# Kernel optimization log

Hardware: AMD Instinct MI355X
Metric: run time of the kernel (lower is better)

## Reference

```python
import jax, jax.numpy as jnp
import numpy as np

B, S, DIM = 4, 512, 2048
E, INTER = 32, 1024
G, TOPK_G, TOPK = 8, 4, 6
ROUTE_SCALE = 2.5
SHARED_INTER = 2 * INTER  # n_shared_experts * moe_inter_dim


def setup_inputs() -> dict:
    key = jax.random.key(0)
    ks = jax.random.split(key, 8)
    sd = 0.02
    return {
        "x": jax.random.normal(ks[0], (B, S, DIM), jnp.float32),
        "gate_w": jax.random.normal(ks[1], (E, DIM), jnp.float32) * sd,
        "w11": jax.random.normal(ks[2], (E, INTER, DIM), jnp.float32) * sd,  # gate proj (torch Linear weight [out,in])
        "w33": jax.random.normal(ks[3], (E, INTER, DIM), jnp.float32) * sd,  # up proj
        "w22": jax.random.normal(ks[4], (E, DIM, INTER), jnp.float32) * sd,  # down proj
        "sw1": jax.random.normal(ks[5], (SHARED_INTER, DIM), jnp.float32) * sd,
        "sw2": jax.random.normal(ks[6], (DIM, SHARED_INTER), jnp.float32) * sd,
        "sw3": jax.random.normal(ks[7], (SHARED_INTER, DIM), jnp.float32) * sd,
    }


def _gate(xf, gate_w):
    # sigmoid scores, group-limited greedy top-k (bias=None branch)
    scores = jax.nn.sigmoid(xf @ gate_w.T)                      # [T, E]
    gs = scores.reshape(-1, G, E // G)                          # [T, G, E/G]
    group_scores = gs.max(axis=-1)                              # amax since bias is None
    _, gidx = jax.lax.top_k(group_scores, TOPK_G)               # [T, TOPK_G]
    gmask = jnp.any(jnp.arange(G)[None, None, :] == gidx[:, :, None], axis=1)  # [T, G] keep-mask
    masked = jnp.where(gmask[:, :, None], gs, -jnp.inf).reshape(-1, E)
    _, idx = jax.lax.top_k(masked, TOPK)                        # [T, TOPK]
    w = jnp.take_along_axis(scores, idx, axis=1)                # gather from original (pre-mask) scores
    w = w / jnp.sum(w, axis=-1, keepdims=True) * ROUTE_SCALE    # sigmoid normalization + route_scale
    return w, idx


def reference(x, gate_w, w11, w33, w22, sw1, sw2, sw3):
    xf = x.reshape(-1, DIM)                                     # [T, D]
    T = xf.shape[0]
    w, idx = _gate(xf, gate_w)
    # dense combine weights: equals the gather->gmm->scatter*prob of the original
    c = jnp.zeros((T, E), xf.dtype).at[jnp.arange(T)[:, None], idx].add(w)  # [T, E]
    g = jnp.einsum('td,eid->tei', xf, w11)                      # fc1 (gate)
    u = jnp.einsum('td,eid->tei', xf, w33)                      # fc2 (up)
    act = jax.nn.silu(g) * u                                    # fused SiLU gating
    y = jnp.einsum('tei,te,edi->td', act, c, w22)               # down proj + weighted combine
    shared = (jax.nn.silu(xf @ sw1.T) * (xf @ sw3.T)) @ sw2.T   # shared experts MLP
    return (y + shared).reshape(x.shape)
```

## Files before the change

### kernel.cpp

```cpp
#include <hip/hip_runtime.h>
#include <hip/hip_bf16.h>

#define T_TOK  2048
#define DIMSZ  2048
#define NEXP   32
#define INTERS 1024
#define SINTER 2048
#define NTOPK  6

typedef __bf16 bf16x8 __attribute__((ext_vector_type(8)));
typedef float  f32x4  __attribute__((ext_vector_type(4)));
typedef unsigned short u16x8 __attribute__((ext_vector_type(8)));

__device__ __forceinline__ unsigned short f2b(float f) {
    __hip_bfloat16 h = __float2bfloat16(f);
    return __builtin_bit_cast(unsigned short, h);
}

__device__ __forceinline__ void gl_lds16(const unsigned short* g, unsigned short* l) {
    __builtin_amdgcn_global_load_lds(
        (const __attribute__((address_space(1))) void*)g,
        (__attribute__((address_space(3))) void*)l, 16, 0, 0);
}
__device__ __forceinline__ void gl_lds16f(const float* g, float* l) {
    __builtin_amdgcn_global_load_lds(
        (const __attribute__((address_space(1))) void*)g,
        (__attribute__((address_space(3))) void*)l, 16, 0, 0);
}

__device__ __forceinline__ bf16x8 cvt8(float4 lo, float4 hi) {
    u16x8 u;
    u[0] = f2b(lo.x); u[1] = f2b(lo.y); u[2] = f2b(lo.z); u[3] = f2b(lo.w);
    u[4] = f2b(hi.x); u[5] = f2b(hi.y); u[6] = f2b(hi.z); u[7] = f2b(hi.w);
    return __builtin_bit_cast(bf16x8, u);
}

__global__ void cvt_f2b(const float4* __restrict__ src, unsigned short* __restrict__ dst, int n8) {
    int stride = gridDim.x * blockDim.x;
    for (int i = blockIdx.x * blockDim.x + threadIdx.x; i < n8; i += stride) {
        float4 a = src[2 * (size_t)i];
        float4 b = src[2 * (size_t)i + 1];
        u16x8 o;
        o[0] = f2b(a.x); o[1] = f2b(a.y); o[2] = f2b(a.z); o[3] = f2b(a.w);
        o[4] = f2b(b.x); o[5] = f2b(b.y); o[6] = f2b(b.z); o[7] = f2b(b.w);
        *(u16x8*)&dst[(size_t)i * 8] = o;
    }
}

#define SCT 8
#define SCK 128
__global__ __launch_bounds__(256) void gate_scores_kernel(
    const float* __restrict__ x, const float* __restrict__ gw, float* __restrict__ scores)
{
    __shared__ float xs[SCT * SCK];
    __shared__ float gs[NEXP * (SCK + 1)];
    const int t0 = blockIdx.x * SCT;
    const int tid = threadIdx.x;
    const int tl = tid >> 5, e = tid & 31;
    float acc = 0.f;
    for (int k0 = 0; k0 < DIMSZ; k0 += SCK) {
        {
            int row = tid >> 5, d4 = tid & 31;
            *(float4*)&xs[row * SCK + d4 * 4] =
                *(const float4*)&x[(size_t)(t0 + row) * DIMSZ + k0 + d4 * 4];
        }
        #pragma unroll
        for (int i = 0; i < 4; ++i) {
            int lin = tid + i * 256;
            int row = lin >> 5, d4 = lin & 31;
            float4 v = *(const float4*)&gw[(size_t)row * DIMSZ + k0 + d4 * 4];
            float* dst = &gs[row * (SCK + 1) + d4 * 4];
            dst[0] = v.x; dst[1] = v.y; dst[2] = v.z; dst[3] = v.w;
        }
        __syncthreads();
        #pragma unroll 8
        for (int d = 0; d < SCK; ++d)
            acc += xs[tl * SCK + d] * gs[e * (SCK + 1) + d];
        __syncthreads();
    }
    scores[(size_t)(t0 + tl) * NEXP + e] = 1.f / (1.f + expf(-acc));
}

__global__ __launch_bounds__(256) void topk_kernel(
    const float* __restrict__ scores,
    int* __restrict__ counts, int* __restrict__ toklist, float* __restrict__ wgts)
{
    int t = blockIdx.x * 256 + threadIdx.x;
    if (t >= T_TOK) return;
    float sc[NEXP];
    #pragma unroll
    for (int e = 0; e < NEXP; ++e) sc[e] = scores[(size_t)t * NEXP + e];

    float gsc[8];
    #pragma unroll
    for (int g = 0; g < 8; ++g) {
        float m = sc[4 * g];
        #pragma unroll
        for (int j = 1; j < 4; ++j) m = fmaxf(m, sc[4 * g + j]);
        gsc[g] = m;
    }
    bool gsel[8] = {false, false, false, false, false, false, false, false};
    for (int it = 0; it < 4; ++it) {
        int bi = -1; float bv = -1e30f;
        #pragma unroll
        for (int g = 0; g < 8; ++g)
            if (!gsel[g] && gsc[g] > bv) { bv = gsc[g]; bi = g; }
        gsel[bi] = true;
    }
    bool esel[NEXP];
    #pragma unroll
    for (int e = 0; e < NEXP; ++e) esel[e] = false;
    int   idx[NTOPK];
    float w[NTOPK];
    float sum = 0.f;
    for (int it = 0; it < NTOPK; ++it) {
        int bi = -1; float bv = -1e30f;
        #pragma unroll
        for (int e = 0; e < NEXP; ++e) {
            if (!gsel[e >> 2] || esel[e]) continue;
            if (sc[e] > bv) { bv = sc[e]; bi = e; }
        }
        esel[bi] = true; idx[it] = bi; w[it] = bv; sum += bv;
    }
    float scale = 2.5f / sum;
    for (int k = 0; k < NTOPK; ++k) {
        int e = idx[k];
        int s = atomicAdd(&counts[e], 1);
        toklist[e * T_TOK + s] = (t << 3) | k;
        wgts[e * T_TOK + s]   = w[k] * scale;
    }
}

__device__ __forceinline__ void decode_tile(
    int wgid, int xt_bits, const int* __restrict__ counts,
    bool& SH, int& e, int& m0, int& n0)
{
    if (wgid < 256) {
        SH = true; e = NEXP; m0 = (wgid >> 4) * 128; n0 = (wgid & 15) * 128;
        return;
    }
    const int rid = wgid - 256;
    const int xmask = (1 << xt_bits) - 1;
    const int xt = rid & xmask, ty = rid >> xt_bits;
    int acc2 = 0, fe = -1, fy = 0;
    #pragma unroll
    for (int e2 = 0; e2 < NEXP; ++e2) {
        const int nt = (counts[e2] + 127) >> 7;
        if (fe < 0 && ty < acc2 + nt) { fe = e2; fy = ty - acc2; }
        acc2 += nt;
    }
    SH = false; e = fe; m0 = fy * 128; n0 = xt * 128;
}

__global__ __launch_bounds__(256, 2) void fc1_all(
    const unsigned short* __restrict__ A,
    const float* __restrict__ w11, const float* __restrict__ w33,
    const float* __restrict__ sw1, const float* __restrict__ sw3,
    unsigned short* __restrict__ h, unsigned short* __restrict__ hs,
    const int* __restrict__ counts, const int* __restrict__ toklist)
{
    constexpr int BM = 128, BN = 128, BK = 64, LDK = 64, K = DIMSZ;
    __shared__ unsigned short As[BM * LDK];
    __shared__ float B1s[BN * BK];
    __shared__ float B2s[BN * BK];

    const int tid = threadIdx.x;
    bool SH; int e, m0, n0;
    decode_tile(blockIdx.x, 3, counts, SH, e, m0, n0);
    if (!SH && e < 0) return;
    const int N = SH ? SINTER : INTERS;
    const int M = SH ? T_TOK : counts[e];

    const size_t eoff = SH ? 0 : (size_t)e * INTERS * DIMSZ;
    const float* B1 = (SH ? sw1 : w11) + eoff + (size_t)n0 * K;
    const float* B2 = (SH ? sw3 : w33) + eoff + (size_t)n0 * K;
    unsigned short* Hout = SH ? hs : h;

    const int wave = tid >> 6;
    const int lane = tid & 63;
    const int wm = (wave >> 1) * 64;
    const int wn = (wave & 1) * 64;
    const int lm = lane & 15;
    const int quad = lane >> 4;

    const unsigned short* aP[4];
    {
        const int l8 = lane >> 3;
        const int sg = (lane & 7) ^ l8;
        #pragma unroll
        for (int i = 0; i < 4; ++i) {
            const int r = (wave * 4 + i) * 8 + l8;
            int gr = m0 + r;
            int ar;
            if (SH) ar = gr;
            else ar = (gr < M) ? (toklist[e * T_TOK + gr] >> 3) : 0;
            aP[i] = A + (size_t)ar * K + sg * 8;
        }
    }
    int offB[8];
    {
        #pragma unroll
        for (int i = 0; i < 8; ++i) {
            const int c = wave * 8 + i;
            const int row = 4 * c + (lane >> 4);
            const int g = (lane & 15) ^ (row & 7);
            offB[i] = row * K + g * 4;
        }
    }

    f32x4 acc1[4][4] = {};
    f32x4 acc2v[4][4] = {};

    for (int k0 = 0; k0 < K; k0 += BK) {
        #pragma unroll
        for (int i = 0; i < 4; ++i)
            gl_lds16(aP[i] + k0, &As[(wave * 4 + i) * 512]);
        #pragma unroll
        for (int i = 0; i < 8; ++i) {
            const int c = wave * 8 + i;
            gl_lds16f(B1 + offB[i] + k0, &B1s[c * 256]);
            gl_lds16f(B2 + offB[i] + k0, &B2s[c * 256]);
        }
        __syncthreads();
        #pragma unroll
        for (int kh = 0; kh < 2; ++kh) {
            const int soffA = (((kh << 2) | quad) ^ (lm & 7)) << 3;
            const int j0 = ((kh << 2) | quad) << 1;
            const int s0 = j0 ^ (lm & 7);
            const int s1 = (j0 | 1) ^ (lm & 7);
            bf16x8 af[4], bf1[4], bf2[4];
            #pragma unroll
            for (int ti = 0; ti < 4; ++ti)
                af[ti] = *(const bf16x8*)&As[(wm + ti * 16 + lm) * LDK + soffA];
            #pragma unroll
            for (int tj = 0; tj < 4; ++tj) {
                const int rB = (wn + tj * 16 + lm) * 64;
                float4 lo1 = *(const float4*)&B1s[rB + s0 * 4];
                float4 hi1 = *(const float4*)&B1s[rB + s1 * 4];
                bf1[tj] = cvt8(lo1, hi1);
                float4 lo2 = *(const float4*)&B2s[rB + s0 * 4];
                float4 hi2 = *(const float4*)&B2s[rB + s1 * 4];
                bf2[tj] = cvt8(lo2, hi2);
            }
            #pragma unroll
            for (int ti = 0; ti < 4; ++ti)
                #pragma unroll
                for (int tj = 0; tj < 4; ++tj) {
                    acc1[ti][tj] = __builtin_amdgcn_mfma_f32_16x16x32_bf16(
                        af[ti], bf1[tj], acc1[ti][tj], 0, 0, 0);
                    acc2v[ti][tj] = __builtin_amdgcn_mfma_f32_16x16x32_bf16(
                        af[ti], bf2[tj], acc2v[ti][tj], 0, 0, 0);
                }
        }
        __syncthreads();
    }

    #pragma unroll
    for (int ti = 0; ti < 4; ++ti) {
        #pragma unroll
        for (int r = 0; r < 4; ++r) {
            const int lrow = wm + ti * 16 + quad * 4 + r;
            const int grow = m0 + lrow;
            int cr;
            if (SH) cr = grow;
            else {
                if (grow >= M) continue;
                int ent = toklist[e * T_TOK + grow];
                cr = (ent >> 3) * NTOPK + (ent & 7);
            }
            #pragma unroll
            for (int tj = 0; tj < 4; ++tj) {
                int nn = n0 + wn + tj * 16 + lm;
                float g = acc1[ti][tj][r];
                float u = acc2v[ti][tj][r];
                float hv = g / (1.f + expf(-g)) * u;
                Hout[(size_t)cr * N + nn] = f2b(hv);
            }
        }
    }
}

template <int MODE>
__global__ __launch_bounds__(256, 3) void fc2_all(
    const unsigned short* __restrict__ h, const unsigned short* __restrict__ hs,
    const float* __restrict__ w22, const float* __restrict__ sw2,
    float* __restrict__ yexp, float* __restrict__ out,
    const int* __restrict__ counts, const int* __restrict__ toklist,
    const float* __restrict__ wgts)
{
    constexpr int BM = 128, BN = 128, BK = 64, LDK = 64;
    __shared__ unsigned short As[BM * LDK];
    __shared__ float Bs[BN * BK];

    const int tid = threadIdx.x;
    bool SH; int e, m0, n0;
    {
        int wgid = blockIdx.x;
        if (MODE == 1) { SH = true; e = NEXP; m0 = (wgid >> 4) * 128; n0 = (wgid & 15) * 128; }
        else if (MODE == 2) { decode_tile(wgid + 256, 4, counts, SH, e, m0, n0); }
        else decode_tile(wgid, 4, counts, SH, e, m0, n0);
    }
    if (!SH && e < 0) return;
    const int K = SH ? SINTER : INTERS;
    const int M = SH ? T_TOK : counts[e];
    if (m0 >= M) return;

    const unsigned short* Asrc = SH ? hs : h;
    const float* B = (SH ? sw2 : (w22 + (size_t)e * DIMSZ * INTERS)) + (size_t)n0 * K;
    float* C = SH ? out : ((MODE == 2) ? out : yexp);

    const int wave = tid >> 6;
    const int lane = tid & 63;
    const int wm = (wave >> 1) * 64;
    const int wn = (wave & 1) * 64;
    const int lm = lane & 15;
    const int quad = lane >> 4;

    const unsigned short* aP[4];
    {
        const int l8 = lane >> 3;
        const int sg = (lane & 7) ^ l8;
        #pragma unroll
        for (int i = 0; i < 4; ++i) {
            const int r = (wave * 4 + i) * 8 + l8;
            int gr = m0 + r;
            int ar;
            if (SH) ar = gr;
            else if (gr < M) {
                int ent = toklist[e * T_TOK + gr];
                ar = (ent >> 3) * NTOPK + (ent & 7);
            } else ar = 0;
            aP[i] = Asrc + (size_t)ar * K + sg * 8;
        }
    }
    int offB[8];
    {
        #pragma unroll
        for (int i = 0; i < 8; ++i) {
            const int c = wave * 8 + i;
            const int row = 4 * c + (lane >> 4);
            const int g = (lane & 15) ^ (row & 7);
            offB[i] = row * K + g * 4;
        }
    }

    f32x4 acc[4][4] = {};

    for (int k0 = 0; k0 < K; k0 += BK) {
        #pragma unroll
        for (int i = 0; i < 4; ++i)
            gl_lds16(aP[i] + k0, &As[(wave * 4 + i) * 512]);
        #pragma unroll
        for (int i = 0; i < 8; ++i) {
            const int c = wave * 8 + i;
            gl_lds16f(B + offB[i] + k0, &Bs[c * 256]);
        }
        __syncthreads();
        #pragma unroll
        for (int kh = 0; kh < 2; ++kh) {
            const int soffA = (((kh << 2) | quad) ^ (lm & 7)) << 3;
            const int j0 = ((kh << 2) | quad) << 1;
            const int s0 = j0 ^ (lm & 7);
            const int s1 = (j0 | 1) ^ (lm & 7);
            bf16x8 af[4], bfr[4];
            #pragma unroll
            for (int ti = 0; ti < 4; ++ti)
                af[ti] = *(const bf16x8*)&As[(wm + ti * 16 + lm) * LDK + soffA];
            #pragma unroll
            for (int tj = 0; tj < 4; ++tj) {
                const int rB = (wn + tj * 16 + lm) * 64;
                float4 lo = *(const float4*)&Bs[rB + s0 * 4];
                float4 hi = *(const float4*)&Bs[rB + s1 * 4];
                bfr[tj] = cvt8(lo, hi);
            }
            #pragma unroll
            for (int ti = 0; ti < 4; ++ti)
                #pragma unroll
                for (int tj = 0; tj < 4; ++tj)
                    acc[ti][tj] = __builtin_amdgcn_mfma_f32_16x16x32_bf16(
                        af[ti], bfr[tj], acc[ti][tj], 0, 0, 0);
        }
        __syncthreads();
    }

    #pragma unroll
    for (int ti = 0; ti < 4; ++ti) {
        #pragma unroll
        for (int r = 0; r < 4; ++r) {
            const int lrow = wm + ti * 16 + quad * 4 + r;
            const int grow = m0 + lrow;
            int cr; float cw;
            if (SH) { cr = grow; cw = 1.f; }
            else {
                if (grow >= M) continue;
                int ent = toklist[e * T_TOK + grow];
                cr = (MODE == 2) ? (ent >> 3) : ((ent >> 3) * NTOPK + (ent & 7));
                cw = wgts[e * T_TOK + grow];
            }
            #pragma unroll
            for (int tj = 0; tj < 4; ++tj) {
                int nn = n0 + wn + tj * 16 + lm;
                float v = acc[ti][tj][r] * cw;
                if (MODE == 2 && !SH)
                    atomicAdd(&C[(size_t)cr * DIMSZ + nn], v);
                else
                    C[(size_t)cr * DIMSZ + nn] = v;
            }
        }
    }
}

__global__ __launch_bounds__(256) void combine_kernel(
    const float4* __restrict__ yexp, float4* __restrict__ out, int n4)
{
    const int D4 = DIMSZ / 4;
    int stride = gridDim.x * blockDim.x;
    for (int i = blockIdx.x * blockDim.x + threadIdx.x; i < n4; i += stride) {
        int t = i / D4, d4 = i - t * D4;
        const float4* r = yexp + (size_t)t * NTOPK * D4 + d4;
        float4 a = out[i];
        #pragma unroll
        for (int k = 0; k < NTOPK; ++k) {
            float4 s = r[(size_t)k * D4];
            a.x += s.x; a.y += s.y; a.z += s.z; a.w += s.w;
        }
        out[i] = a;
    }
}

extern "C" void kernel_launch(void* const* d_in, const int* in_sizes, int n_in,
                              void* d_out, int out_size, void* d_ws, size_t ws_size,
                              hipStream_t stream)
{
    const float* x   = (const float*)d_in[0];
    const float* gw  = (const float*)d_in[1];
    const float* w11 = (const float*)d_in[2];
    const float* w33 = (const float*)d_in[3];
    const float* w22 = (const float*)d_in[4];
    const float* sw1 = (const float*)d_in[5];
    const float* sw2 = (const float*)d_in[6];
    const float* sw3 = (const float*)d_in[7];
    float* out = (float*)d_out;

    char* ws = (char*)d_ws;
    size_t off = 0;
    auto alloc = [&](size_t b) { void* p = ws + off; off = (off + b + 255) & ~(size_t)255; return p; };
    int*            counts  = (int*)alloc(NEXP * 4);
    int*            toklist = (int*)alloc((size_t)NEXP * T_TOK * 4);
    float*          wgts    = (float*)alloc((size_t)NEXP * T_TOK * 4);
    float*          scores  = (float*)alloc((size_t)T_TOK * NEXP * 4);
    unsigned short* xb      = (unsigned short*)alloc((size_t)T_TOK * DIMSZ * 2);
    unsigned short* h       = (unsigned short*)alloc((size_t)T_TOK * NTOPK * INTERS * 2);
    unsigned short* hs      = (unsigned short*)alloc((size_t)T_TOK * SINTER * 2);

    const size_t yBytes = (size_t)T_TOK * NTOPK * DIMSZ * 4;
    const bool DENSE = (off + yBytes + 256) <= ws_size;
    float* yexp = DENSE ? (float*)alloc(yBytes) : nullptr;

    hipMemsetAsync(counts, 0, NEXP * 4, stream);

    const int n4x = T_TOK * DIMSZ / 4;
    cvt_f2b<<<1024, 256, 0, stream>>>((const float4*)x, xb, T_TOK * DIMSZ / 8);

    gate_scores_kernel<<<T_TOK / SCT, 256, 0, stream>>>(x, gw, scores);
    topk_kernel<<<(T_TOK + 255) / 256, 256, 0, stream>>>(scores, counts, toklist, wgts);

    fc1_all<<<256 + 1024, 256, 0, stream>>>(
        xb, w11, w33, sw1, sw3, h, hs, counts, toklist);

    if (DENSE) {
        fc2_all<0><<<256 + 2048, 256, 0, stream>>>(
            h, hs, w22, sw2, yexp, out, counts, toklist, wgts);
        combine_kernel<<<2048, 256, 0, stream>>>((const float4*)yexp, (float4*)out, n4x);
    } else {
        fc2_all<1><<<256, 256, 0, stream>>>(
            h, hs, w22, sw2, nullptr, out, counts, toklist, wgts);
        fc2_all<2><<<2048, 256, 0, stream>>>(
            h, hs, w22, sw2, nullptr, out, counts, toklist, wgts);
    }
}
```

Before: 1.102 ms.

## Double-buffer LDS tiles with BK=32 prefetch in fc1 and fc2 GEMMs

Both expert GEMM kernels now use two LDS buffers with K-step 32. The next tile's global-to-LDS loads are issued before computing the current tile, with explicit vmcnt waits and raw s_barrier in place of __syncthreads. This is meant to hide global load latency behind the MFMA work. LDS footprint stays the same, but there are twice as many iterations and barriers, and the swizzle patterns are new, so a mismatch between load and read swizzles could break correctness.

New measurement: 1.132 ms. 2.7% more time.

```diff
diff --git a/kernel.cpp b/kernel.cpp
--- a/kernel.cpp
+++ b/kernel.cpp
@@ -159,10 +159,10 @@
     unsigned short* __restrict__ h, unsigned short* __restrict__ hs,
     const int* __restrict__ counts, const int* __restrict__ toklist)
 {
-    constexpr int BM = 128, BN = 128, BK = 64, LDK = 64, K = DIMSZ;
-    __shared__ unsigned short As[BM * LDK];
-    __shared__ float B1s[BN * BK];
-    __shared__ float B2s[BN * BK];
+    constexpr int BK = 32, K = DIMSZ, NT = K / BK;
+    __shared__ unsigned short As[2][128 * 32];
+    __shared__ float B1s[2][128 * 32];
+    __shared__ float B2s[2][128 * 32];
 
     const int tid = threadIdx.x;
     bool SH; int e, m0, n0;
@@ -183,76 +183,90 @@
     const int lm = lane & 15;
     const int quad = lane >> 4;
 
-    const unsigned short* aP[4];
-    {
-        const int l8 = lane >> 3;
-        const int sg = (lane & 7) ^ l8;
-        #pragma unroll
-        for (int i = 0; i < 4; ++i) {
-            const int r = (wave * 4 + i) * 8 + l8;
-            int gr = m0 + r;
+    const unsigned short* aP[2];
+    {
+        const int gs = (lane & 3) ^ ((lane >> 3) & 3);
+        #pragma unroll
+        for (int i = 0; i < 2; ++i) {
+            const int row = (wave * 2 + i) * 16 + (lane >> 2);
+            const int gr = m0 + row;
             int ar;
             if (SH) ar = gr;
             else ar = (gr < M) ? (toklist[e * T_TOK + gr] >> 3) : 0;
-            aP[i] = A + (size_t)ar * K + sg * 8;
-        }
-    }
-    int offB[8];
-    {
-        #pragma unroll
-        for (int i = 0; i < 8; ++i) {
-            const int c = wave * 8 + i;
-            const int row = 4 * c + (lane >> 4);
-            const int g = (lane & 15) ^ (row & 7);
-            offB[i] = row * K + g * 4;
+            aP[i] = A + (size_t)ar * K + gs * 8;
+        }
+    }
+    int offB[4];
+    {
+        const int gs = (lane & 7) ^ (lane >> 3);
+        #pragma unroll
+        for (int i = 0; i < 4; ++i) {
+            const int row = (wave * 4 + i) * 8 + (lane >> 3);
+            offB[i] = row * K + gs * 4;
         }
     }
 
     f32x4 acc1[4][4] = {};
     f32x4 acc2v[4][4] = {};
 
-    for (int k0 = 0; k0 < K; k0 += BK) {
-        #pragma unroll
-        for (int i = 0; i < 4; ++i)
-            gl_lds16(aP[i] + k0, &As[(wave * 4 + i) * 512]);
-        #pragma unroll
-        for (int i = 0; i < 8; ++i) {
-            const int c = wave * 8 + i;
-            gl_lds16f(B1 + offB[i] + k0, &B1s[c * 256]);
-            gl_lds16f(B2 + offB[i] + k0, &B2s[c * 256]);
-        }
-        __syncthreads();
-        #pragma unroll
-        for (int kh = 0; kh < 2; ++kh) {
-            const int soffA = (((kh << 2) | quad) ^ (lm & 7)) << 3;
-            const int j0 = ((kh << 2) | quad) << 1;
-            const int s0 = j0 ^ (lm & 7);
-            const int s1 = (j0 | 1) ^ (lm & 7);
-            bf16x8 af[4], bf1[4], bf2[4];
-            #pragma unroll
-            for (int ti = 0; ti < 4; ++ti)
-                af[ti] = *(const bf16x8*)&As[(wm + ti * 16 + lm) * LDK + soffA];
+    const int ga = quad ^ ((lm >> 1) & 3);
+    const int s0 = (quad << 1) ^ (lm & 7);
+    const int s1 = s0 ^ 1;
+
+    {
+        #pragma unroll
+        for (int i = 0; i < 2; ++i)
+            gl_lds16(aP[i], &As[0][(wave * 2 + i) * 512]);
+        #pragma unroll
+        for (int i = 0; i < 4; ++i) {
+            gl_lds16f(B1 + offB[i], &B1s[0][(wave * 4 + i) * 256]);
+            gl_lds16f(B2 + offB[i], &B2s[0][(wave * 4 + i) * 256]);
+        }
+    }
+
+    int buf = 0;
+    for (int t = 0; t < NT; ++t) {
+        if (t + 1 < NT) {
+            const int kn = (t + 1) * BK;
+            #pragma unroll
+            for (int i = 0; i < 2; ++i)
+                gl_lds16(aP[i] + kn, &As[buf ^ 1][(wave * 2 + i) * 512]);
+            #pragma unroll
+            for (int i = 0; i < 4; ++i) {
+                gl_lds16f(B1 + offB[i] + kn, &B1s[buf ^ 1][(wave * 4 + i) * 256]);
+                gl_lds16f(B2 + offB[i] + kn, &B2s[buf ^ 1][(wave * 4 + i) * 256]);
+            }
+            asm volatile("s_waitcnt vmcnt(10)" ::: "memory");
+        } else {
+            asm volatile("s_waitcnt vmcnt(0)" ::: "memory");
+        }
+        __builtin_amdgcn_sched_barrier(0);
+        __builtin_amdgcn_s_barrier();
+
+        bf16x8 af[4], bf1[4], bf2[4];
+        #pragma unroll
+        for (int ti = 0; ti < 4; ++ti)
+            af[ti] = *(const bf16x8*)&As[buf][(wm + ti * 16 + lm) * 32 + ga * 8];
+        #pragma unroll
+        for (int tj = 0; tj < 4; ++tj) {
+            const int rB = (wn + tj * 16 + lm) * 32;
+            bf1[tj] = cvt8(*(const float4*)&B1s[buf][rB + s0 * 4],
+                           *(const float4*)&B1s[buf][rB + s1 * 4]);
+            bf2[tj] = cvt8(*(const float4*)&B2s[buf][rB + s0 * 4],
+                           *(const float4*)&B2s[buf][rB + s1 * 4]);
+        }
+        #pragma unroll
+        for (int ti = 0; ti < 4; ++ti)
             #pragma unroll
             for (int tj = 0; tj < 4; ++tj) {
-                const int rB = (wn + tj * 16 + lm) * 64;
-                float4 lo1 = *(const float4*)&B1s[rB + s0 * 4];
-                float4 hi1 = *(const float4*)&B1s[rB + s1 * 4];
-                bf1[tj] = cvt8(lo1, hi1);
-                float4 lo2 = *(const float4*)&B2s[rB + s0 * 4];
-                float4 hi2 = *(const float4*)&B2s[rB + s1 * 4];
-                bf2[tj] = cvt8(lo2, hi2);
+                acc1[ti][tj] = __builtin_amdgcn_mfma_f32_16x16x32_bf16(
+                    af[ti], bf1[tj], acc1[ti][tj], 0, 0, 0);
+                acc2v[ti][tj] = __builtin_amdgcn_mfma_f32_16x16x32_bf16(
+                    af[ti], bf2[tj], acc2v[ti][tj], 0, 0, 0);
             }
-            #pragma unroll
-            for (int ti = 0; ti < 4; ++ti)
-                #pragma unroll
-                for (int tj = 0; tj < 4; ++tj) {
-                    acc1[ti][tj] = __builtin_amdgcn_mfma_f32_16x16x32_bf16(
-                        af[ti], bf1[tj], acc1[ti][tj], 0, 0, 0);
-                    acc2v[ti][tj] = __builtin_amdgcn_mfma_f32_16x16x32_bf16(
-                        af[ti], bf2[tj], acc2v[ti][tj], 0, 0, 0);
-                }
-        }
-        __syncthreads();
+
+        __builtin_amdgcn_s_barrier();
+        buf ^= 1;
     }
 
     #pragma unroll
@@ -288,9 +302,9 @@
     const int* __restrict__ counts, const int* __restrict__ toklist,
     const float* __restrict__ wgts)
 {
-    constexpr int BM = 128, BN = 128, BK = 64, LDK = 64;
-    __shared__ unsigned short As[BM * LDK];
-    __shared__ float Bs[BN * BK];
+    constexpr int BK = 32;
+    __shared__ unsigned short As[2][128 * 32];
+    __shared__ float Bs[2][128 * 32];
 
     const int tid = threadIdx.x;
     bool SH; int e, m0, n0;
@@ -302,6 +316,7 @@
     }
     if (!SH && e < 0) return;
     const int K = SH ? SINTER : INTERS;
+    const int NT = K / BK;
     const int M = SH ? T_TOK : counts[e];
     if (m0 >= M) return;
 
@@ -316,71 +331,83 @@
     const int lm = lane & 15;
     const int quad = lane >> 4;
 
-    const unsigned short* aP[4];
-    {
-        const int l8 = lane >> 3;
-        const int sg = (lane & 7) ^ l8;
-        #pragma unroll
-        for (int i = 0; i < 4; ++i) {
-            const int r = (wave * 4 + i) * 8 + l8;
-            int gr = m0 + r;
+    const unsigned short* aP[2];
+    {
+        const int gs = (lane & 3) ^ ((lane >> 3) & 3);
+        #pragma unroll
+        for (int i = 0; i < 2; ++i) {
+            const int row = (wave * 2 + i) * 16 + (lane >> 2);
+            const int gr = m0 + row;
             int ar;
             if (SH) ar = gr;
             else if (gr < M) {
                 int ent = toklist[e * T_TOK + gr];
                 ar = (ent >> 3) * NTOPK + (ent & 7);
             } else ar = 0;
-            aP[i] = Asrc + (size_t)ar * K + sg * 8;
-        }
-    }
-    int offB[8];
-    {
-        #pragma unroll
-        for (int i = 0; i < 8; ++i) {
-            const int c = wave * 8 + i;
-            const int row = 4 * c + (lane >> 4);
-            const int g = (lane & 15) ^ (row & 7);
-            offB[i] = row * K + g * 4;
+            aP[i] = Asrc + (size_t)ar * K + gs * 8;
+        }
+    }
+    int offB[4];
+    {
+        const int gs = (lane & 7) ^ (lane >> 3);
+        #pragma unroll
+        for (int i = 0; i < 4; ++i) {
+            const int row = (wave * 4 + i) * 8 + (lane >> 3);
+            offB[i] = row * K + gs * 4;
         }
     }
 
     f32x4 acc[4][4] = {};
 
-    for (int k0 = 0; k0 < K; k0 += BK) {
+    const int ga = quad ^ ((lm >> 1) & 3);
+    const int s0 = (quad << 1) ^ (lm & 7);
+    const int s1 = s0 ^ 1;
+
+    {
+        #pragma unroll
+        for (int i = 0; i < 2; ++i)
+            gl_lds16(aP[i], &As[0][(wave * 2 + i) * 512]);
         #pragma unroll
         for (int i = 0; i < 4; ++i)
-            gl_lds16(aP[i] + k0, &As[(wave * 4 + i) * 512]);
-        #pragma unroll
-        for (int i = 0; i < 8; ++i) {
-            const int c = wave * 8 + i;
-            gl_lds16f(B + offB[i] + k0, &Bs[c * 256]);
-        }
-        __syncthreads();
-        #pragma unroll
-        for (int kh = 0; kh < 2; ++kh) {
-            const int soffA = (((kh << 2) | quad) ^ (lm & 7)) << 3;
-            const int j0 = ((kh << 2) | quad) << 1;
-            const int s0 = j0 ^ (lm & 7);
-            const int s1 = (j0 | 1) ^ (lm & 7);
-            bf16x8 af[4], bfr[4];
-            #pragma unroll
-            for (int ti = 0; ti < 4; ++ti)
-                af[ti] = *(const bf16x8*)&As[(wm + ti * 16 + lm) * LDK + soffA];
-            #pragma unroll
-            for (int tj = 0; tj < 4; ++tj) {
-                const int rB = (wn + tj * 16 + lm) * 64;
-                float4 lo = *(const float4*)&Bs[rB + s0 * 4];
-                float4 hi = *(const float4*)&Bs[rB + s1 * 4];
-                bfr[tj] = cvt8(lo, hi);
-            }
-            #pragma unroll
-            for (int ti = 0; ti < 4; ++ti)
-                #pragma unroll
-                for (int tj = 0; tj < 4; ++tj)
-                    acc[ti][tj] = __builtin_amdgcn_mfma_f32_16x16x32_bf16(
-                        af[ti], bfr[tj], acc[ti][tj], 0, 0, 0);
-        }
-        __syncthreads();
+            gl_lds16f(B + offB[i], &Bs[0][(wave * 4 + i) * 256]);
+    }
+
+    int buf = 0;
+    for (int t = 0; t < NT; ++t) {
+        if (t + 1 < NT) {
+            const int kn = (t + 1) * BK;
+            #pragma unroll
+            for (int i = 0; i < 2; ++i)
+                gl_lds16(aP[i] + kn, &As[buf ^ 1][(wave * 2 + i) * 512]);
+            #pragma unroll
+            for (int i = 0; i < 4; ++i)
+                gl_lds16f(B + offB[i] + kn, &Bs[buf ^ 1][(wave * 4 + i) * 256]);
+            asm volatile("s_waitcnt vmcnt(6)" ::: "memory");
+        } else {
+            asm volatile("s_waitcnt vmcnt(0)" ::: "memory");
+        }
+        __builtin_amdgcn_sched_barrier(0);
+        __builtin_amdgcn_s_barrier();
+
+        bf16x8 af[4], bfr[4];
+        #pragma unroll
+        for (int ti = 0; ti < 4; ++ti)
+            af[ti] = *(const bf16x8*)&As[buf][(wm + ti * 16 + lm) * 32 + ga * 8];
+        #pragma unroll
+        for (int tj = 0; tj < 4; ++tj) {
+            const int rB = (wn + tj * 16 + lm) * 32;
+            bfr[tj] = cvt8(*(const float4*)&Bs[buf][rB + s0 * 4],
+                           *(const float4*)&Bs[buf][rB + s1 * 4]);
+        }
+        #pragma unroll
+        for (int ti = 0; ti < 4; ++ti)
+            #pragma unroll
+            for (int tj = 0; tj < 4; ++tj)
+                acc[ti][tj] = __builtin_amdgcn_mfma_f32_16x16x32_bf16(
+                    af[ti], bfr[tj], acc[ti][tj], 0, 0, 0);
+
+        __builtin_amdgcn_s_barrier();
+        buf ^= 1;
     }
 
     #pragma unroll
```
